# Optimization experiments

Measured on AMD Instinct MI355X. Metric: run time of the kernel, lower is better.

## Reference

```python
import jax, jax.numpy as jnp
import numpy as np

EPS = 1e-6
NUM_STAGES = 7
NUM_FILTERS = 8


def _gaussian_kernel(size=5, sigma=1.0):
    ax = np.arange(size) - (size - 1) / 2.0
    g = np.exp(-(ax ** 2) / (2.0 * sigma ** 2))
    k = np.outer(g, g)
    k = k / k.sum()
    return jnp.asarray(k, dtype=jnp.float32).reshape(1, 1, size, size)


def _refl_conv(x, k, p):
    # reflect-pad then VALID correlation (matches F.pad(mode='reflect') + F.conv2d)
    xp = jnp.pad(x, ((0, 0), (0, 0), (p, p), (p, p)), mode='reflect')
    return jax.lax.conv_general_dilated(xp, k, (1, 1), 'VALID',
                                        dimension_numbers=('NCHW', 'OIHW', 'NCHW'))


def setup_inputs() -> dict:
    key = jax.random.key(0)
    k1, k2, k3, k4 = jax.random.split(key, 4)
    B, H, W = 8, 512, 512
    noisy = jax.random.uniform(k1, (B, 1, H, W), dtype=jnp.float32, minval=0.05, maxval=1.0)
    # per-stage fixed analysis filters (buffer in torch): randn / sqrt(k*k)
    filters = jax.random.normal(k2, (NUM_STAGES, NUM_FILTERS, 1, 3, 3), dtype=jnp.float32) / 3.0
    # depthwise 1x1 influence projection: weight + bias per channel per stage
    w = jax.random.normal(k3, (NUM_STAGES, NUM_FILTERS), dtype=jnp.float32)
    b = jax.random.normal(k4, (NUM_STAGES, NUM_FILTERS), dtype=jnp.float32) * 0.1
    lam = jnp.full((NUM_STAGES,), 0.1, dtype=jnp.float32)
    gate = jnp.full((NUM_STAGES,), -2.0, dtype=jnp.float32)
    gauss = _gaussian_kernel(5, 1.0)
    return {"noisy": noisy, "filters": filters, "w": w, "b": b,
            "lam": lam, "gate": gate, "gauss": gauss, "looks": 4}


def reference(noisy, filters, w, b, lam, gate, gauss, looks):
    del looks  # unused when use_level_embedding=False
    est = noisy  # initial_estimate is identity
    for s in range(filters.shape[0]):
        f = filters[s]  # [C,1,3,3]
        # u_sigma: 5x5 gaussian smoothing with reflect padding
        u_sigma = _refl_conv(est, gauss, 2)
        iw = jnp.maximum(
            u_sigma / jnp.maximum(jnp.max(u_sigma, axis=(2, 3), keepdims=True), EPS),
            EPS)  # [B,1,H,W]
        # analysis conv: 1 -> C channels
        resp = _refl_conv(est, f, 1)  # [B,C,H,W]
        # depthwise 1x1 conv + tanh influence
        infl = jnp.tanh(resp * w[s][None, :, None, None] + b[s][None, :, None, None])
        z = iw * infl
        # conv_transpose2d(z, flip(f), padding=1) == conv2d(z, f^T as (1,C,3,3), zero pad 1)
        diff = jax.lax.conv_general_dilated(
            z, jnp.transpose(f, (1, 0, 2, 3)), (1, 1), ((1, 1), (1, 1)),
            dimension_numbers=('NCHW', 'OIHW', 'NCHW'))  # [B,1,H,W]
        fidelity_grad = (est - noisy) / (est * est + EPS)
        est2 = est - diff - lam[s] * iw * fidelity_grad
        g = jax.nn.sigmoid(gate[s])
        est = jnp.clip(est2 + g * (noisy - est2), EPS, 1.0)
    return jnp.clip(est, EPS, 1.0)
```

## Files before the change

### kernel.cpp

```cpp
#include <hip/hip_runtime.h>
#include <hip/hip_bf16.h>

#define EPS 1e-6f
#define H 512
#define W 512
#define NB 8
#define NC 8
#define NS 7
#define LOG2E 1.4426950408889634f

__device__ __forceinline__ int refl(int t, int n) {
    if (t < 0) t = -t;
    if (t >= n) t = 2 * n - 2 - t;
    return t;
}

#define GW 256
#define GR 32
#define NBLK ((W / GW) * (H / GR))

__global__ __launch_bounds__(256) void gauss_max_kernel(
    const float* __restrict__ est, const float* __restrict__ gauss,
    float* __restrict__ blockmax)
{
    const int tx = threadIdx.x, ty = threadIdx.y;
    const int x0 = blockIdx.x * GW;
    const int R  = blockIdx.y * GR + ty * 8;
    const int b  = blockIdx.z;
    const float* e = est + (size_t)b * H * W;
    const int c0 = x0 + tx * 4;

    const float g0 = sqrtf(gauss[0]);
    const float g1 = sqrtf(gauss[6]);
    const float g2 = sqrtf(gauss[12]);

    float4 h0, h1, h2, h3, h4;
    float m = 0.f;

#pragma unroll
    for (int k = 0; k < 12; k++) {
        const float* row = e + refl(R - 2 + k, H) * W;
        float4 v = *(const float4*)&row[c0];
        float em2 = __shfl_up(v.z, 1);
        float em1 = __shfl_up(v.w, 1);
        float ep1 = __shfl_down(v.x, 1);
        float ep2 = __shfl_down(v.y, 1);
        if (tx == 0) {
            if (x0 == 0) { em2 = v.z; em1 = v.y; }
            else         { em2 = row[c0 - 2]; em1 = row[c0 - 1]; }
        }
        if (tx == 63) {
            if (x0 + GW == W) { ep1 = v.z; ep2 = v.y; }
            else              { ep1 = row[c0 + 4]; ep2 = row[c0 + 5]; }
        }
        float4 hc;
        hc.x = g0 * (em2 + v.z) + g1 * (em1 + v.y) + g2 * v.x;
        hc.y = g0 * (em1 + v.w) + g1 * (v.x + v.z) + g2 * v.y;
        hc.z = g0 * (v.x + ep1) + g1 * (v.y + v.w) + g2 * v.z;
        hc.w = g0 * (v.y + ep2) + g1 * (v.z + ep1) + g2 * v.w;
        h0 = h1; h1 = h2; h2 = h3; h3 = h4; h4 = hc;
        if (k >= 4) {
            float ux = g0 * (h0.x + h4.x) + g1 * (h1.x + h3.x) + g2 * h2.x;
            float uy = g0 * (h0.y + h4.y) + g1 * (h1.y + h3.y) + g2 * h2.y;
            float uz = g0 * (h0.z + h4.z) + g1 * (h1.z + h3.z) + g2 * h2.z;
            float uw = g0 * (h0.w + h4.w) + g1 * (h1.w + h3.w) + g2 * h2.w;
            m = fmaxf(m, fmaxf(fmaxf(ux, uy), fmaxf(uz, uw)));
        }
    }

#pragma unroll
    for (int off = 32; off > 0; off >>= 1)
        m = fmaxf(m, __shfl_xor(m, off, 64));
    __shared__ float wm[4];
    if (tx == 0) wm[ty] = m;
    __syncthreads();
    if (tx == 0 && ty == 0) {
        float mm = fmaxf(fmaxf(wm[0], wm[1]), fmaxf(wm[2], wm[3]));
        blockmax[b * NBLK + blockIdx.y * gridDim.x + blockIdx.x] = mm;
    }
}

#define TX 64
#define TY 16
#define ZW 66
#define ZH 18
#define ZP 67
#define EW 70
#define EH 22
#define EP 71
#define HW_ 66
#define HH 22

__global__ __launch_bounds__(256) void stage_kernel(
    const float* __restrict__ est, const float* __restrict__ noisy,
    const float* __restrict__ blockmax,
    const float* __restrict__ filt,
    const float* __restrict__ wv, const float* __restrict__ bv,
    const float* __restrict__ lamp, const float* __restrict__ gatep,
    const float* __restrict__ gauss,
    float* __restrict__ out)
{
    __shared__ float esh[EH][EP];
    __shared__ float ush[ZH][ZP];
    __shared__ float zsh[NC][ZH][ZP];
    __shared__ float fsh[NC][9];
    __shared__ float wsh[NC], bsh[NC];

    const int tx = threadIdx.x, ty = threadIdx.y;
    const int tid = ty * 64 + tx;
    const int x0 = blockIdx.x * TX, y0 = blockIdx.y * TY;
    const int b = blockIdx.z;
    const float* e  = est   + (size_t)b * H * W;
    const float* nz = noisy + (size_t)b * H * W;

    if (tid < 72) fsh[tid / 9][tid % 9] = filt[tid];
    else if (tid < 80) {
        int c = tid - 72;
        wsh[c] = wv[c] * (2.f * LOG2E);
        bsh[c] = bv[c] * (2.f * LOG2E);
    }

    const float g0 = sqrtf(gauss[0]);
    const float g1 = sqrtf(gauss[6]);
    const float g2 = sqrtf(gauss[12]);

    float m = blockmax[b * NBLK + (tid & 31)];
#pragma unroll
    for (int off = 16; off > 0; off >>= 1)
        m = fmaxf(m, __shfl_xor(m, off, 64));
    const float dinv = __builtin_amdgcn_rcpf(fmaxf(m, EPS));

    const float lam = lamp[0];
    const float g = __builtin_amdgcn_rcpf(1.f + __builtin_amdgcn_exp2f(-gatep[0] * LOG2E));

    for (int i = tid; i < EH * EW; i += 256) {
        int ly = i / EW, lx = i % EW;
        esh[ly][lx] = e[refl(y0 + ly - 3, H) * W + refl(x0 + lx - 3, W)];
    }
    __syncthreads();

    float* hb = &zsh[0][0][0];
    for (int i = tid; i < HH * HW_; i += 256) {
        int ly = i / HW_, lx = i % HW_;
        hb[ly * ZP + lx] = g0 * (esh[ly][lx] + esh[ly][lx + 4])
                         + g1 * (esh[ly][lx + 1] + esh[ly][lx + 3])
                         + g2 * esh[ly][lx + 2];
    }
    __syncthreads();

    for (int i = tid; i < ZH * ZW; i += 256) {
        int ly = i / ZW, lx = i % ZW;
        float us = g0 * (hb[ly * ZP + lx] + hb[(ly + 4) * ZP + lx])
                 + g1 * (hb[(ly + 1) * ZP + lx] + hb[(ly + 3) * ZP + lx])
                 + g2 * hb[(ly + 2) * ZP + lx];
        int gy = y0 + ly - 1, gx = x0 + lx - 1;
        bool valid = (gy >= 0 && gy < H && gx >= 0 && gx < W);
        ush[ly][lx] = valid ? fmaxf(us * dinv, EPS) : 0.f;
    }
    __syncthreads();

    for (int i = tid; i < ZH * ZW; i += 256) {
        int ly = i / ZW, lx = i % ZW;
        float iw = ush[ly][lx];
        float ew[9];
#pragma unroll
        for (int dy = 0; dy < 3; dy++)
#pragma unroll
            for (int dx = 0; dx < 3; dx++)
                ew[dy * 3 + dx] = esh[ly + 1 + dy][lx + 1 + dx];
#pragma unroll
        for (int c = 0; c < NC; c++) {
            float r = 0.f;
#pragma unroll
            for (int k = 0; k < 9; k++) r += ew[k] * fsh[c][k];
            float a = __builtin_amdgcn_exp2f(r * wsh[c] + bsh[c]);
            float t = 1.f - 2.f * __builtin_amdgcn_rcpf(a + 1.f);
            zsh[c][ly][lx] = iw * t;
        }
    }
    __syncthreads();

    const int r0 = ty * 4;
    float acc0 = 0.f, acc1 = 0.f, acc2 = 0.f, acc3 = 0.f;
#pragma unroll
    for (int c = 0; c < NC; c++) {
        float f0 = fsh[c][0], f1 = fsh[c][1], f2 = fsh[c][2];
        float f3 = fsh[c][3], f4 = fsh[c][4], f5 = fsh[c][5];
        float f6 = fsh[c][6], f7 = fsh[c][7], f8 = fsh[c][8];
        float a0 = zsh[c][r0 + 0][tx], a1 = zsh[c][r0 + 0][tx + 1], a2 = zsh[c][r0 + 0][tx + 2];
        float b0 = zsh[c][r0 + 1][tx], b1 = zsh[c][r0 + 1][tx + 1], b2 = zsh[c][r0 + 1][tx + 2];
        float c0 = zsh[c][r0 + 2][tx], c1 = zsh[c][r0 + 2][tx + 1], c2 = zsh[c][r0 + 2][tx + 2];
        acc0 += f0*a0 + f1*a1 + f2*a2 + f3*b0 + f4*b1 + f5*b2 + f6*c0 + f7*c1 + f8*c2;
        float d0 = zsh[c][r0 + 3][tx], d1 = zsh[c][r0 + 3][tx + 1], d2 = zsh[c][r0 + 3][tx + 2];
        acc1 += f0*b0 + f1*b1 + f2*b2 + f3*c0 + f4*c1 + f5*c2 + f6*d0 + f7*d1 + f8*d2;
        float e0 = zsh[c][r0 + 4][tx], e1 = zsh[c][r0 + 4][tx + 1], e2 = zsh[c][r0 + 4][tx + 2];
        acc2 += f0*c0 + f1*c1 + f2*c2 + f3*d0 + f4*d1 + f5*d2 + f6*e0 + f7*e1 + f8*e2;
        float h0 = zsh[c][r0 + 5][tx], h1 = zsh[c][r0 + 5][tx + 1], h2 = zsh[c][r0 + 5][tx + 2];
        acc3 += f0*d0 + f1*d1 + f2*d2 + f3*e0 + f4*e1 + f5*e2 + f6*h0 + f7*h1 + f8*h2;
    }

    float accs[4] = {acc0, acc1, acc2, acc3};
#pragma unroll
    for (int rr = 0; rr < 4; rr++) {
        const int oy = r0 + rr;
        float eo = esh[oy + 3][tx + 3];
        float n0 = nz[(size_t)(y0 + oy) * W + x0 + tx];
        float iwc = ush[oy + 1][tx + 1];
        float fg = (eo - n0) * __builtin_amdgcn_rcpf(eo * eo + EPS);
        float est2 = eo - accs[rr] - lam * iwc * fg;
        float en = est2 + g * (n0 - est2);
        en = fminf(fmaxf(en, EPS), 1.f);
        out[(size_t)b * H * W + (size_t)(y0 + oy) * W + x0 + tx] = en;
    }
}

extern "C" void kernel_launch(void* const* d_in, const int* in_sizes, int n_in,
                              void* d_out, int out_size, void* d_ws, size_t ws_size,
                              hipStream_t stream)
{
    const float* noisy   = (const float*)d_in[0];
    const float* filters = (const float*)d_in[1];
    const float* wv      = (const float*)d_in[2];
    const float* bv      = (const float*)d_in[3];
    const float* lam     = (const float*)d_in[4];
    const float* gate    = (const float*)d_in[5];
    const float* gauss   = (const float*)d_in[6];
    float* out = (float*)d_out;

    char* ws = (char*)d_ws;
    float* ws0      = (float*)ws;
    float* blockmax = (float*)(ws + (8u << 20));

    const float* cur = noisy;
    for (int s = 0; s < NS; s++) {
        float* nxt = (s % 2 == 0) ? out : ws0;
        gauss_max_kernel<<<dim3(W / GW, H / GR, NB), dim3(64, 4), 0, stream>>>(
            cur, gauss, blockmax);
        stage_kernel<<<dim3(W / TX, H / TY, NB), dim3(64, 4), 0, stream>>>(
            cur, noisy, blockmax,
            filters + s * NC * 9, wv + s * NC, bv + s * NC, lam + s, gate + s, gauss, nxt);
        cur = nxt;
    }
}
```

Before: 325.2 us.

## Use channel-interleaved z layout and packed float2 math in stage kernel

Changes the shared z buffer from channel-major to pixel-major with channels innermost, transposes the filter table, and rewrites the analysis and transpose-conv loops to use two-wide float vectors so packed FMA instructions can be emitted. The transpose conv now computes a 2x2 output block per thread, reusing each loaded z vector across several taps, and stores outputs as float2. The Gaussian passes are also vectorised two pixels at a time, with padding widened to even sizes for aligned 8-byte LDS access. This aims to cut VALU and LDS instruction counts, but the new pixel-major layout and 8-byte strides may introduce LDS bank conflicts and raise register pressure.

```diff
diff --git a/kernel.cpp b/kernel.cpp
--- a/kernel.cpp
+++ b/kernel.cpp
@@ -8,6 +8,9 @@
 #define NC 8
 #define NS 7
 #define LOG2E 1.4426950408889634f
+
+typedef float v2f __attribute__((ext_vector_type(2)));
+__device__ __forceinline__ v2f sp(float s) { return (v2f){s, s}; }
 
 __device__ __forceinline__ int refl(int t, int n) {
     if (t < 0) t = -t;
@@ -84,10 +87,10 @@
 #define TY 16
 #define ZW 66
 #define ZH 18
-#define ZP 67
+#define ZP 68
 #define EW 70
 #define EH 22
-#define EP 71
+#define EP 72
 #define HW_ 66
 #define HH 22
 
@@ -102,9 +105,9 @@
 {
     __shared__ float esh[EH][EP];
     __shared__ float ush[ZH][ZP];
-    __shared__ float zsh[NC][ZH][ZP];
-    __shared__ float fsh[NC][9];
-    __shared__ float wsh[NC], bsh[NC];
+    __shared__ float zsh[ZH][ZP][NC];
+    __shared__ float fshP[9][NC];
+    __shared__ float wshP[NC], bshP[NC];
 
     const int tx = threadIdx.x, ty = threadIdx.y;
     const int tid = ty * 64 + tx;
@@ -113,11 +116,11 @@
     const float* e  = est   + (size_t)b * H * W;
     const float* nz = noisy + (size_t)b * H * W;
 
-    if (tid < 72) fsh[tid / 9][tid % 9] = filt[tid];
+    if (tid < 72) fshP[tid % 9][tid / 9] = filt[tid];
     else if (tid < 80) {
         int c = tid - 72;
-        wsh[c] = wv[c] * (2.f * LOG2E);
-        bsh[c] = bv[c] * (2.f * LOG2E);
+        wshP[c] = wv[c] * (2.f * LOG2E);
+        bshP[c] = bv[c] * (2.f * LOG2E);
     }
 
     const float g0 = sqrtf(gauss[0]);
@@ -140,22 +143,33 @@
     __syncthreads();
 
     float* hb = &zsh[0][0][0];
-    for (int i = tid; i < HH * HW_; i += 256) {
-        int ly = i / HW_, lx = i % HW_;
-        hb[ly * ZP + lx] = g0 * (esh[ly][lx] + esh[ly][lx + 4])
-                         + g1 * (esh[ly][lx + 1] + esh[ly][lx + 3])
-                         + g2 * esh[ly][lx + 2];
-    }
-    __syncthreads();
-
-    for (int i = tid; i < ZH * ZW; i += 256) {
-        int ly = i / ZW, lx = i % ZW;
-        float us = g0 * (hb[ly * ZP + lx] + hb[(ly + 4) * ZP + lx])
-                 + g1 * (hb[(ly + 1) * ZP + lx] + hb[(ly + 3) * ZP + lx])
-                 + g2 * hb[(ly + 2) * ZP + lx];
+    for (int i = tid; i < HH * 33; i += 256) {
+        int ly = i / 33, lx = 2 * (i % 33);
+        v2f a = *(const v2f*)&esh[ly][lx];
+        v2f bb = *(const v2f*)&esh[ly][lx + 2];
+        v2f c = *(const v2f*)&esh[ly][lx + 4];
+        v2f s04 = a + c;
+        v2f s13 = (v2f){a.y, bb.x} + (v2f){bb.y, c.x};
+        v2f u = sp(g0) * s04 + sp(g1) * s13 + sp(g2) * bb;
+        *(v2f*)&hb[ly * ZP + lx] = u;
+    }
+    __syncthreads();
+
+    for (int i = tid; i < ZH * 33; i += 256) {
+        int ly = i / 33, lx = 2 * (i % 33);
+        v2f h0v = *(const v2f*)&hb[(ly + 0) * ZP + lx];
+        v2f h1v = *(const v2f*)&hb[(ly + 1) * ZP + lx];
+        v2f h2v = *(const v2f*)&hb[(ly + 2) * ZP + lx];
+        v2f h3v = *(const v2f*)&hb[(ly + 3) * ZP + lx];
+        v2f h4v = *(const v2f*)&hb[(ly + 4) * ZP + lx];
+        v2f u = sp(g0) * (h0v + h4v) + sp(g1) * (h1v + h3v) + sp(g2) * h2v;
+        u = u * sp(dinv);
+        u.x = fmaxf(u.x, EPS); u.y = fmaxf(u.y, EPS);
         int gy = y0 + ly - 1, gx = x0 + lx - 1;
-        bool valid = (gy >= 0 && gy < H && gx >= 0 && gx < W);
-        ush[ly][lx] = valid ? fmaxf(us * dinv, EPS) : 0.f;
+        bool vy = (gy >= 0 && gy < H);
+        float o0 = (vy && gx >= 0     && gx < W)     ? u.x : 0.f;
+        float o1 = (vy && gx + 1 >= 0 && gx + 1 < W) ? u.y : 0.f;
+        *(v2f*)&ush[ly][lx] = (v2f){o0, o1};
     }
     __syncthreads();
 
@@ -168,49 +182,99 @@
 #pragma unroll
             for (int dx = 0; dx < 3; dx++)
                 ew[dy * 3 + dx] = esh[ly + 1 + dy][lx + 1 + dx];
-#pragma unroll
-        for (int c = 0; c < NC; c++) {
-            float r = 0.f;
-#pragma unroll
-            for (int k = 0; k < 9; k++) r += ew[k] * fsh[c][k];
-            float a = __builtin_amdgcn_exp2f(r * wsh[c] + bsh[c]);
-            float t = 1.f - 2.f * __builtin_amdgcn_rcpf(a + 1.f);
-            zsh[c][ly][lx] = iw * t;
-        }
-    }
-    __syncthreads();
-
-    const int r0 = ty * 4;
-    float acc0 = 0.f, acc1 = 0.f, acc2 = 0.f, acc3 = 0.f;
-#pragma unroll
-    for (int c = 0; c < NC; c++) {
-        float f0 = fsh[c][0], f1 = fsh[c][1], f2 = fsh[c][2];
-        float f3 = fsh[c][3], f4 = fsh[c][4], f5 = fsh[c][5];
-        float f6 = fsh[c][6], f7 = fsh[c][7], f8 = fsh[c][8];
-        float a0 = zsh[c][r0 + 0][tx], a1 = zsh[c][r0 + 0][tx + 1], a2 = zsh[c][r0 + 0][tx + 2];
-        float b0 = zsh[c][r0 + 1][tx], b1 = zsh[c][r0 + 1][tx + 1], b2 = zsh[c][r0 + 1][tx + 2];
-        float c0 = zsh[c][r0 + 2][tx], c1 = zsh[c][r0 + 2][tx + 1], c2 = zsh[c][r0 + 2][tx + 2];
-        acc0 += f0*a0 + f1*a1 + f2*a2 + f3*b0 + f4*b1 + f5*b2 + f6*c0 + f7*c1 + f8*c2;
-        float d0 = zsh[c][r0 + 3][tx], d1 = zsh[c][r0 + 3][tx + 1], d2 = zsh[c][r0 + 3][tx + 2];
-        acc1 += f0*b0 + f1*b1 + f2*b2 + f3*c0 + f4*c1 + f5*c2 + f6*d0 + f7*d1 + f8*d2;
-        float e0 = zsh[c][r0 + 4][tx], e1 = zsh[c][r0 + 4][tx + 1], e2 = zsh[c][r0 + 4][tx + 2];
-        acc2 += f0*c0 + f1*c1 + f2*c2 + f3*d0 + f4*d1 + f5*d2 + f6*e0 + f7*e1 + f8*e2;
-        float h0 = zsh[c][r0 + 5][tx], h1 = zsh[c][r0 + 5][tx + 1], h2 = zsh[c][r0 + 5][tx + 2];
-        acc3 += f0*d0 + f1*d1 + f2*d2 + f3*e0 + f4*e1 + f5*e2 + f6*h0 + f7*h1 + f8*h2;
-    }
-
-    float accs[4] = {acc0, acc1, acc2, acc3};
-#pragma unroll
-    for (int rr = 0; rr < 4; rr++) {
-        const int oy = r0 + rr;
-        float eo = esh[oy + 3][tx + 3];
-        float n0 = nz[(size_t)(y0 + oy) * W + x0 + tx];
-        float iwc = ush[oy + 1][tx + 1];
-        float fg = (eo - n0) * __builtin_amdgcn_rcpf(eo * eo + EPS);
-        float est2 = eo - accs[rr] - lam * iwc * fg;
-        float en = est2 + g * (n0 - est2);
-        en = fminf(fmaxf(en, EPS), 1.f);
-        out[(size_t)b * H * W + (size_t)(y0 + oy) * W + x0 + tx] = en;
+        v2f r[4] = {sp(0.f), sp(0.f), sp(0.f), sp(0.f)};
+#pragma unroll
+        for (int k = 0; k < 9; k++) {
+            const v2f* fp = (const v2f*)&fshP[k][0];
+            v2f es = sp(ew[k]);
+            r[0] += es * fp[0];
+            r[1] += es * fp[1];
+            r[2] += es * fp[2];
+            r[3] += es * fp[3];
+        }
+        float* zp = &zsh[ly][lx][0];
+#pragma unroll
+        for (int j = 0; j < 4; j++) {
+            const v2f* wp = (const v2f*)&wshP[0];
+            const v2f* bp = (const v2f*)&bshP[0];
+            v2f wr = wp[j] * r[j] + bp[j];
+            float a0 = __builtin_amdgcn_exp2f(wr.x);
+            float a1 = __builtin_amdgcn_exp2f(wr.y);
+            float t0 = 1.f - 2.f * __builtin_amdgcn_rcpf(a0 + 1.f);
+            float t1 = 1.f - 2.f * __builtin_amdgcn_rcpf(a1 + 1.f);
+            *(v2f*)(zp + 2 * j) = sp(iw) * (v2f){t0, t1};
+        }
+    }
+    __syncthreads();
+
+    const int p = tid & 31;
+    const int r0 = (tid >> 5) * 2;
+    const int xc = 2 * p;
+
+    v2f fr[9][4];
+#pragma unroll
+    for (int k = 0; k < 9; k++)
+#pragma unroll
+        for (int j = 0; j < 4; j++)
+            fr[k][j] = *(const v2f*)&fshP[k][2 * j];
+
+    v2f acc[2][2][4];
+#pragma unroll
+    for (int a = 0; a < 2; a++)
+#pragma unroll
+        for (int c = 0; c < 2; c++)
+#pragma unroll
+            for (int j = 0; j < 4; j++)
+                acc[a][c][j] = sp(0.f);
+
+#pragma unroll
+    for (int dr = 0; dr < 4; dr++) {
+#pragma unroll
+        for (int dc = 0; dc < 4; dc++) {
+            const float* zp = &zsh[r0 + dr][xc + dc][0];
+            v2f zv0 = *(const v2f*)(zp + 0);
+            v2f zv1 = *(const v2f*)(zp + 2);
+            v2f zv2 = *(const v2f*)(zp + 4);
+            v2f zv3 = *(const v2f*)(zp + 6);
+#pragma unroll
+            for (int orow = 0; orow < 2; orow++) {
+                int ky = dr - orow;
+                if (ky < 0 || ky > 2) continue;
+#pragma unroll
+                for (int ocol = 0; ocol < 2; ocol++) {
+                    int kx = dc - ocol;
+                    if (kx < 0 || kx > 2) continue;
+                    int tap = ky * 3 + kx;
+                    acc[orow][ocol][0] += zv0 * fr[tap][0];
+                    acc[orow][ocol][1] += zv1 * fr[tap][1];
+                    acc[orow][ocol][2] += zv2 * fr[tap][2];
+                    acc[orow][ocol][3] += zv3 * fr[tap][3];
+                }
+            }
+        }
+    }
+
+#pragma unroll
+    for (int orow = 0; orow < 2; orow++) {
+        const int r = r0 + orow;
+        const int y = y0 + r;
+        v2f n2 = *(const v2f*)&nz[(size_t)y * W + x0 + xc];
+        v2f res;
+#pragma unroll
+        for (int ocol = 0; ocol < 2; ocol++) {
+            v2f s = (acc[orow][ocol][0] + acc[orow][ocol][1])
+                  + (acc[orow][ocol][2] + acc[orow][ocol][3]);
+            float diff = s.x + s.y;
+            float eo = esh[r + 3][xc + 3 + ocol];
+            float n0 = (ocol == 0) ? n2.x : n2.y;
+            float iwc = ush[r + 1][xc + 1 + ocol];
+            float fg = (eo - n0) * __builtin_amdgcn_rcpf(eo * eo + EPS);
+            float est2 = eo - diff - lam * iwc * fg;
+            float en = est2 + g * (n0 - est2);
+            en = fminf(fmaxf(en, EPS), 1.f);
+            if (ocol == 0) res.x = en; else res.y = en;
+        }
+        *(v2f*)&out[(size_t)b * H * W + (size_t)y * W + x0 + xc] = res;
     }
 }
 
```

Result: slower. 371.2 us (+14.1%).

## Rewrite stage kernel as register-streaming single-wavefront column sweep with shuffles

Applied to the files above, without the earlier changes.

The stage kernel drops its shared-memory tiles and becomes a one-wavefront block. Each lane owns one column of a 58-wide band and streams down a 16-row slab, keeping a rolling window of rows and separable Gaussian partial sums in registers. Horizontal neighbours come from lane shuffles, and the transposed convolution is accumulated through per-row partial sums passed between lanes and rows. This removes LDS traffic and barriers, at the cost of recomputing halo columns (6 of 64 lanes), a serial row dependence, and high register use for the 72 filter coefficients.

```diff
diff --git a/kernel.cpp b/kernel.cpp
--- a/kernel.cpp
+++ b/kernel.cpp
@@ -80,18 +80,11 @@
     }
 }
 
-#define TX 64
-#define TY 16
-#define ZW 66
-#define ZH 18
-#define ZP 67
-#define EW 70
-#define EH 22
-#define EP 71
-#define HW_ 66
-#define HH 22
-
-__global__ __launch_bounds__(256) void stage_kernel(
+#define SLAB 16
+#define BANDW 58
+#define NBANDS 9
+
+__global__ __launch_bounds__(64) void stage_kernel(
     const float* __restrict__ est, const float* __restrict__ noisy,
     const float* __restrict__ blockmax,
     const float* __restrict__ filt,
@@ -100,117 +93,122 @@
     const float* __restrict__ gauss,
     float* __restrict__ out)
 {
-    __shared__ float esh[EH][EP];
-    __shared__ float ush[ZH][ZP];
-    __shared__ float zsh[NC][ZH][ZP];
-    __shared__ float fsh[NC][9];
-    __shared__ float wsh[NC], bsh[NC];
-
-    const int tx = threadIdx.x, ty = threadIdx.y;
-    const int tid = ty * 64 + tx;
-    const int x0 = blockIdx.x * TX, y0 = blockIdx.y * TY;
+    const int l = threadIdx.x;
+    const int band = blockIdx.x;
+    const int R = blockIdx.y * SLAB;
     const int b = blockIdx.z;
-    const float* e  = est   + (size_t)b * H * W;
-    const float* nz = noisy + (size_t)b * H * W;
-
-    if (tid < 72) fsh[tid / 9][tid % 9] = filt[tid];
-    else if (tid < 80) {
-        int c = tid - 72;
-        wsh[c] = wv[c] * (2.f * LOG2E);
-        bsh[c] = bv[c] * (2.f * LOG2E);
-    }
-
+    const int c = band * BANDW - 3 + l;
+    const int cl = refl(c, W);
+    const int ccl = c < 0 ? 0 : (c > W - 1 ? W - 1 : c);
+
+    const float* e   = est   + (size_t)b * H * W;
+    const float* nz  = noisy + (size_t)b * H * W;
+    float*       op  = out   + (size_t)b * H * W;
+
+    float fco[NC][9];
+#pragma unroll
+    for (int ch = 0; ch < NC; ch++)
+#pragma unroll
+        for (int k = 0; k < 9; k++) fco[ch][k] = filt[ch * 9 + k];
+    float w2[NC], b2[NC];
+#pragma unroll
+    for (int ch = 0; ch < NC; ch++) {
+        w2[ch] = wv[ch] * (2.f * LOG2E);
+        b2[ch] = bv[ch] * (2.f * LOG2E);
+    }
     const float g0 = sqrtf(gauss[0]);
     const float g1 = sqrtf(gauss[6]);
     const float g2 = sqrtf(gauss[12]);
-
-    float m = blockmax[b * NBLK + (tid & 31)];
+    const float lam = lamp[0];
+    const float g = __builtin_amdgcn_rcpf(1.f + __builtin_amdgcn_exp2f(-gatep[0] * LOG2E));
+
+    float m = blockmax[b * NBLK + (l & 31)];
 #pragma unroll
     for (int off = 16; off > 0; off >>= 1)
         m = fmaxf(m, __shfl_xor(m, off, 64));
     const float dinv = __builtin_amdgcn_rcpf(fmaxf(m, EPS));
 
-    const float lam = lamp[0];
-    const float g = __builtin_amdgcn_rcpf(1.f + __builtin_amdgcn_exp2f(-gatep[0] * LOG2E));
-
-    for (int i = tid; i < EH * EW; i += 256) {
-        int ly = i / EW, lx = i % EW;
-        esh[ly][lx] = e[refl(y0 + ly - 3, H) * W + refl(x0 + lx - 3, W)];
-    }
-    __syncthreads();
-
-    float* hb = &zsh[0][0][0];
-    for (int i = tid; i < HH * HW_; i += 256) {
-        int ly = i / HW_, lx = i % HW_;
-        hb[ly * ZP + lx] = g0 * (esh[ly][lx] + esh[ly][lx + 4])
-                         + g1 * (esh[ly][lx + 1] + esh[ly][lx + 3])
-                         + g2 * esh[ly][lx + 2];
-    }
-    __syncthreads();
-
-    for (int i = tid; i < ZH * ZW; i += 256) {
-        int ly = i / ZW, lx = i % ZW;
-        float us = g0 * (hb[ly * ZP + lx] + hb[(ly + 4) * ZP + lx])
-                 + g1 * (hb[(ly + 1) * ZP + lx] + hb[(ly + 3) * ZP + lx])
-                 + g2 * hb[(ly + 2) * ZP + lx];
-        int gy = y0 + ly - 1, gx = x0 + lx - 1;
-        bool valid = (gy >= 0 && gy < H && gx >= 0 && gx < W);
-        ush[ly][lx] = valid ? fmaxf(us * dinv, EPS) : 0.f;
-    }
-    __syncthreads();
-
-    for (int i = tid; i < ZH * ZW; i += 256) {
-        int ly = i / ZW, lx = i % ZW;
-        float iw = ush[ly][lx];
-        float ew[9];
-#pragma unroll
-        for (int dy = 0; dy < 3; dy++)
-#pragma unroll
-            for (int dx = 0; dx < 3; dx++)
-                ew[dy * 3 + dx] = esh[ly + 1 + dy][lx + 1 + dx];
-#pragma unroll
-        for (int c = 0; c < NC; c++) {
-            float r = 0.f;
-#pragma unroll
-            for (int k = 0; k < 9; k++) r += ew[k] * fsh[c][k];
-            float a = __builtin_amdgcn_exp2f(r * wsh[c] + bsh[c]);
-            float t = 1.f - 2.f * __builtin_amdgcn_rcpf(a + 1.f);
-            zsh[c][ly][lx] = iw * t;
-        }
-    }
-    __syncthreads();
-
-    const int r0 = ty * 4;
-    float acc0 = 0.f, acc1 = 0.f, acc2 = 0.f, acc3 = 0.f;
-#pragma unroll
-    for (int c = 0; c < NC; c++) {
-        float f0 = fsh[c][0], f1 = fsh[c][1], f2 = fsh[c][2];
-        float f3 = fsh[c][3], f4 = fsh[c][4], f5 = fsh[c][5];
-        float f6 = fsh[c][6], f7 = fsh[c][7], f8 = fsh[c][8];
-        float a0 = zsh[c][r0 + 0][tx], a1 = zsh[c][r0 + 0][tx + 1], a2 = zsh[c][r0 + 0][tx + 2];
-        float b0 = zsh[c][r0 + 1][tx], b1 = zsh[c][r0 + 1][tx + 1], b2 = zsh[c][r0 + 1][tx + 2];
-        float c0 = zsh[c][r0 + 2][tx], c1 = zsh[c][r0 + 2][tx + 1], c2 = zsh[c][r0 + 2][tx + 2];
-        acc0 += f0*a0 + f1*a1 + f2*a2 + f3*b0 + f4*b1 + f5*b2 + f6*c0 + f7*c1 + f8*c2;
-        float d0 = zsh[c][r0 + 3][tx], d1 = zsh[c][r0 + 3][tx + 1], d2 = zsh[c][r0 + 3][tx + 2];
-        acc1 += f0*b0 + f1*b1 + f2*b2 + f3*c0 + f4*c1 + f5*c2 + f6*d0 + f7*d1 + f8*d2;
-        float e0 = zsh[c][r0 + 4][tx], e1 = zsh[c][r0 + 4][tx + 1], e2 = zsh[c][r0 + 4][tx + 2];
-        acc2 += f0*c0 + f1*c1 + f2*c2 + f3*d0 + f4*d1 + f5*d2 + f6*e0 + f7*e1 + f8*e2;
-        float h0 = zsh[c][r0 + 5][tx], h1 = zsh[c][r0 + 5][tx + 1], h2 = zsh[c][r0 + 5][tx + 2];
-        acc3 += f0*d0 + f1*d1 + f2*d2 + f3*e0 + f4*e1 + f5*e2 + f6*h0 + f7*h1 + f8*h2;
-    }
-
-    float accs[4] = {acc0, acc1, acc2, acc3};
-#pragma unroll
-    for (int rr = 0; rr < 4; rr++) {
-        const int oy = r0 + rr;
-        float eo = esh[oy + 3][tx + 3];
-        float n0 = nz[(size_t)(y0 + oy) * W + x0 + tx];
-        float iwc = ush[oy + 1][tx + 1];
-        float fg = (eo - n0) * __builtin_amdgcn_rcpf(eo * eo + EPS);
-        float est2 = eo - accs[rr] - lam * iwc * fg;
-        float en = est2 + g * (n0 - est2);
-        en = fminf(fmaxf(en, EPS), 1.f);
-        out[(size_t)b * H * W + (size_t)(y0 + oy) * W + x0 + tx] = en;
+    const bool cm0 = (c == 0), cm1 = (c == 1), cp0 = (c == W - 1), cp1 = (c == W - 2);
+    const bool c_in = (c >= 0) && (c < W);
+    const bool c_st = (l >= 3) && (l <= 60) && (c < W);
+
+    auto loadrow = [&](int vr, float& v, float& m1, float& p1, float& hv) {
+        v = e[(size_t)refl(vr, H) * W + cl];
+        float m1r = __shfl_up(v, 1), p1r = __shfl_down(v, 1);
+        float m2r = __shfl_up(v, 2), p2r = __shfl_down(v, 2);
+        m1 = cm0 ? p1r : m1r;
+        float m2 = cm0 ? p2r : (cm1 ? v : m2r);
+        p1 = cp0 ? m1r : p1r;
+        float p2 = cp0 ? m2r : (cp1 ? v : p2r);
+        hv = g0 * (m2 + p2) + g1 * (m1 + p1) + g2 * v;
+    };
+
+    float ev[4], em[4], ep[4];
+    float h[5];
+
+    {
+        float v, m1, p1, hv;
+        loadrow(R - 3, v, m1, p1, hv); h[1] = hv;
+        loadrow(R - 2, v, m1, p1, hv); h[2] = hv; ev[1] = v; em[1] = m1; ep[1] = p1;
+        loadrow(R - 1, v, m1, p1, hv); h[3] = hv; ev[2] = v; em[2] = m1; ep[2] = p1;
+        loadrow(R - 0, v, m1, p1, hv); h[4] = hv; ev[3] = v; em[3] = m1; ep[3] = p1;
+    }
+    ev[0] = 0.f; em[0] = 0.f; ep[0] = 0.f; h[0] = 0.f;
+
+    float acc0 = 0.f, acc1 = 0.f, iw_prev = 0.f;
+
+#pragma unroll 3
+    for (int i = 0; i < SLAB + 2; ++i) {
+        const int t = R - 1 + i;
+
+        float v, m1, p1, hnew;
+        loadrow(t + 2, v, m1, p1, hnew);
+
+        const int orow = t - 1 < 0 ? 0 : (t - 1 > H - 1 ? H - 1 : t - 1);
+        const float n0 = nz[(size_t)orow * W + ccl];
+
+        h[0] = h[1]; h[1] = h[2]; h[2] = h[3]; h[3] = h[4]; h[4] = hnew;
+        float iw = g0 * (h[0] + h[4]) + g1 * (h[1] + h[3]) + g2 * h[2];
+        iw = fmaxf(iw * dinv, EPS);
+        if (!c_in || t < 0 || t > H - 1) iw = 0.f;
+
+        ev[0] = ev[1]; em[0] = em[1]; ep[0] = ep[1];
+        ev[1] = ev[2]; em[1] = em[2]; ep[1] = ep[2];
+        ev[2] = ev[3]; em[2] = em[3]; ep[2] = ep[3];
+        ev[3] = v;     em[3] = m1;    ep[3] = p1;
+
+        float U0 = 0.f, U1 = 0.f, U2 = 0.f;
+        float V0 = 0.f, V1 = 0.f, V2 = 0.f;
+        float W0 = 0.f, W1 = 0.f, W2 = 0.f;
+#pragma unroll
+        for (int ch = 0; ch < NC; ch++) {
+            float r = fco[ch][0] * em[0] + fco[ch][1] * ev[0] + fco[ch][2] * ep[0]
+                    + fco[ch][3] * em[1] + fco[ch][4] * ev[1] + fco[ch][5] * ep[1]
+                    + fco[ch][6] * em[2] + fco[ch][7] * ev[2] + fco[ch][8] * ep[2];
+            float a = __builtin_amdgcn_exp2f(r * w2[ch] + b2[ch]);
+            float z = iw * (1.f - 2.f * __builtin_amdgcn_rcpf(a + 1.f));
+            U0 += fco[ch][0] * z; V0 += fco[ch][1] * z; W0 += fco[ch][2] * z;
+            U1 += fco[ch][3] * z; V1 += fco[ch][4] * z; W1 += fco[ch][5] * z;
+            U2 += fco[ch][6] * z; V2 += fco[ch][7] * z; W2 += fco[ch][8] * z;
+        }
+
+        float q0 = __shfl_up(U0, 1) + V0 + __shfl_down(W0, 1);
+        float q1 = __shfl_up(U1, 1) + V1 + __shfl_down(W1, 1);
+        float q2 = __shfl_up(U2, 1) + V2 + __shfl_down(W2, 1);
+
+        float diff = acc0 + q2;
+        acc0 = acc1 + q1;
+        acc1 = q0;
+
+        if (i >= 2 && c_st) {
+            float eo = ev[0];
+            float fg = (eo - n0) * __builtin_amdgcn_rcpf(eo * eo + EPS);
+            float est2 = eo - diff - lam * iw_prev * fg;
+            float en = est2 + g * (n0 - est2);
+            en = fminf(fmaxf(en, EPS), 1.f);
+            op[(size_t)(t - 1) * W + c] = en;
+        }
+        iw_prev = iw;
     }
 }
 
@@ -236,7 +234,7 @@
         float* nxt = (s % 2 == 0) ? out : ws0;
         gauss_max_kernel<<<dim3(W / GW, H / GR, NB), dim3(64, 4), 0, stream>>>(
             cur, gauss, blockmax);
-        stage_kernel<<<dim3(W / TX, H / TY, NB), dim3(64, 4), 0, stream>>>(
+        stage_kernel<<<dim3(NBANDS, H / SLAB, NB), dim3(64), 0, stream>>>(
             cur, noisy, blockmax,
             filters + s * NC * 9, wv + s * NC, bv + s * NC, lam + s, gate + s, gauss, nxt);
         cur = nxt;
```

New measurement: 417.1 us. 28.2% more time.
